# Kernel optimization log

Hardware: AMD Instinct MI355X
Metric: run time of the kernel (lower is better)

The kernel has to match this reference:

```python
import jax, jax.numpy as jnp
import numpy as np


def setup_inputs() -> dict:
    key = jax.random.key(0)
    k1, k2 = jax.random.split(key)
    B, N, P = 8, 16384, 2048
    xyz = jax.random.uniform(k1, (B, N, 3), dtype=jnp.float32)
    center_xyz = jax.random.uniform(k2, (B, P, 3), dtype=jnp.float32)
    return {
        "xyz": xyz,
        "center_xyz": center_xyz,
        "max_radius": jnp.float32(0.2),
        "sample_num": 32,
    }


def reference(xyz, center_xyz, max_radius, sample_num):
    # xyz: [B, N, 3], center_xyz: [B, P, 3] -> idx: [B, P, sample_num] int32
    B, P, _ = center_xyz.shape
    N = xyz.shape[1]
    S = int(sample_num)

    # squared distances via ||c||^2 + ||x||^2 - 2 c.x (avoids [B,P,N,3] temp)
    xn = jnp.sum(xyz * xyz, axis=-1)                      # [B, N]
    cn = jnp.sum(center_xyz * center_xyz, axis=-1)        # [B, P]
    dot = jnp.einsum("bpd,bnd->bpn", center_xyz, xyz)     # [B, P, N]
    d2 = cn[:, :, None] + xn[:, None, :] - 2.0 * dot       # [B, P, N]

    mask = d2 < (max_radius * max_radius)                  # dist < r  <=>  dist^2 < r^2
    # rank of each point among the valid ones (in index order), as in torch.where order
    rank = jnp.cumsum(mask.astype(jnp.int32), axis=-1) - 1 # [B, P, N]
    take = mask & (rank < S)
    # valid points write into slot=rank; everything else into dump slot S (discarded)
    slot = jnp.where(take, rank, S)                        # [B, P, N]

    buf = jnp.zeros((B, P, S + 1), dtype=jnp.int32)        # zeros match torch init fill
    bi = jnp.arange(B)[:, None, None]
    pi = jnp.arange(P)[None, :, None]
    src = jnp.broadcast_to(jnp.arange(N, dtype=jnp.int32), (B, P, N))
    buf = buf.at[bi, pi, slot].set(src)
    return buf[:, :, :S]
```

## Files before the change

kernel.cpp:

```cpp
#include <hip/hip_runtime.h>
#include <hip/hip_bf16.h>


__global__ __launch_bounds__(256) void ball_query_kernel(
    const float* __restrict__ xyz,
    const float* __restrict__ center,
    const float* __restrict__ p_radius,
    const int*   __restrict__ p_sample,
    int* __restrict__ out,
    int B, int N, int P)
{
    const int S = p_sample[0];
    const float r = p_radius[0];
    const float r2 = __fmul_rn(r, r);

    const int wave_id = (blockIdx.x * blockDim.x + threadIdx.x) >> 6;
    const int lane = threadIdx.x & 63;
    const int total_waves = B * P;
    if (wave_id >= total_waves) return;

    const int b = wave_id / P;
    const int p = wave_id - b * P;

    const float cx = center[(size_t)(b * P + p) * 3 + 0];
    const float cy = center[(size_t)(b * P + p) * 3 + 1];
    const float cz = center[(size_t)(b * P + p) * 3 + 2];
    const float cn = __builtin_fmaf(cz, cz,
                      __builtin_fmaf(cy, cy, __fmul_rn(cx, cx)));

    const float* xb = xyz + (size_t)b * N * 3;
    int* ob = out + (size_t)(b * P + p) * S;

    int cnt = 0;
    for (int n0 = 0; n0 < N && cnt < S; n0 += 256) {
        float px[4], py[4], pz[4];
#pragma unroll
        for (int j = 0; j < 4; ++j) {
            const int n = n0 + j * 64 + lane;
            px[j] = xb[(size_t)n * 3 + 0];
            py[j] = xb[(size_t)n * 3 + 1];
            pz[j] = xb[(size_t)n * 3 + 2];
        }
#pragma unroll
        for (int j = 0; j < 4; ++j) {
            const float x = px[j], y = py[j], z = pz[j];
            const float xn = __builtin_fmaf(z, z,
                              __builtin_fmaf(y, y, __fmul_rn(x, x)));
            const float dot = __builtin_fmaf(cz, z,
                               __builtin_fmaf(cy, y, __fmul_rn(cx, x)));
            const float d2 = __fsub_rn(__fadd_rn(cn, xn), __fmul_rn(2.0f, dot));

            const bool valid = d2 < r2;
            const unsigned long long m = __ballot(valid);
            const int rank = __builtin_amdgcn_mbcnt_hi(
                (unsigned)(m >> 32),
                __builtin_amdgcn_mbcnt_lo((unsigned)m, 0u));
            if (valid && (cnt + rank) < S) {
                ob[cnt + rank] = n0 + j * 64 + lane;
            }
            cnt += __popcll(m);
        }
    }

    if (cnt > S) cnt = S;
    for (int s = cnt + lane; s < S; s += 64) {
        ob[s] = 0;
    }
}

extern "C" void kernel_launch(void* const* d_in, const int* in_sizes, int n_in,
                              void* d_out, int out_size, void* d_ws, size_t ws_size,
                              hipStream_t stream) {
    const float* xyz      = (const float*)d_in[0];
    const float* center   = (const float*)d_in[1];
    const float* p_radius = (const float*)d_in[2];
    const int*   p_sample = (const int*)d_in[3];

    const int B = 8;
    const int N = in_sizes[0] / (B * 3);
    const int P = in_sizes[1] / (B * 3);

    int* out = (int*)d_out;

    const int total_waves = B * P;
    const int threads = 256;
    const int blocks = (total_waves * 64 + threads - 1) / threads;

    ball_query_kernel<<<blocks, threads, 0, stream>>>(
        xyz, center, p_radius, p_sample, out, B, N, P);
}
```

Measured before the change: 83.92 us.

## Double-buffer point loads with 8-chunk register prefetch in ball query

Widens each iteration from 4 to 8 point chunks per wave (512 points). It adds two register buffers so the next 512-point block is loaded while the current one is processed. The goal is to hide global-memory latency in the serial early-exit scan. In exchange it uses more registers and may load points past the early-exit point. The tail handling assumes N is a multiple of 512.

```diff
diff --git a/kernel.cpp b/kernel.cpp
--- a/kernel.cpp
+++ b/kernel.cpp
@@ -32,18 +32,25 @@
     int* ob = out + (size_t)(b * P + p) * S;
 
     int cnt = 0;
-    for (int n0 = 0; n0 < N && cnt < S; n0 += 256) {
-        float px[4], py[4], pz[4];
+
+    float Ax[8], Ay[8], Az[8];
+    float Bx[8], By[8], Bz[8];
+
+    auto load8 = [&](float (&X)[8], float (&Y)[8], float (&Z)[8], int m0) {
+        const float* q = xb + (size_t)(m0 + lane) * 3;
 #pragma unroll
-        for (int j = 0; j < 4; ++j) {
-            const int n = n0 + j * 64 + lane;
-            px[j] = xb[(size_t)n * 3 + 0];
-            py[j] = xb[(size_t)n * 3 + 1];
-            pz[j] = xb[(size_t)n * 3 + 2];
+        for (int j = 0; j < 8; ++j) {
+            X[j] = q[j * 192 + 0];
+            Y[j] = q[j * 192 + 1];
+            Z[j] = q[j * 192 + 2];
         }
+    };
+
+    auto process8 = [&](const float (&X)[8], const float (&Y)[8],
+                        const float (&Z)[8], int m0) -> bool {
 #pragma unroll
-        for (int j = 0; j < 4; ++j) {
-            const float x = px[j], y = py[j], z = pz[j];
+        for (int j = 0; j < 8; ++j) {
+            const float x = X[j], y = Y[j], z = Z[j];
             const float xn = __builtin_fmaf(z, z,
                               __builtin_fmaf(y, y, __fmul_rn(x, x)));
             const float dot = __builtin_fmaf(cz, z,
@@ -56,10 +63,24 @@
                 (unsigned)(m >> 32),
                 __builtin_amdgcn_mbcnt_lo((unsigned)m, 0u));
             if (valid && (cnt + rank) < S) {
-                ob[cnt + rank] = n0 + j * 64 + lane;
+                ob[cnt + rank] = m0 + j * 64 + lane;
             }
             cnt += __popcll(m);
         }
+        return cnt >= S;
+    };
+
+    load8(Ax, Ay, Az, 0);
+    int n0 = 0;
+    while (true) {
+        if (n0 + 1024 <= N) load8(Bx, By, Bz, n0 + 512);
+        if (process8(Ax, Ay, Az, n0)) break;
+        n0 += 512;
+        if (n0 >= N) break;
+        if (n0 + 1024 <= N) load8(Ax, Ay, Az, n0 + 512);
+        if (process8(Bx, By, Bz, n0)) break;
+        n0 += 512;
+        if (n0 >= N) break;
     }
 
     if (cnt > S) cnt = S;
```

After: 87.52 us. 1.04x slower.

## Process each center with a full block using cross-wave prefix counts

Applied to the files above, without the earlier changes.

Assigns one 256-thread block per center instead of one wave, so four waves scan 1024 points per iteration and combine their hit counts through a shared-memory prefix with a barrier. This is meant to shorten the serial scan per center before 32 neighbors are found. It adds a barrier per iteration and may scan more points than needed, since the early-exit granularity is now 1024 points.

```diff
diff --git a/kernel.cpp b/kernel.cpp
--- a/kernel.cpp
+++ b/kernel.cpp
@@ -2,7 +2,7 @@
 #include <hip/hip_bf16.h>
 
 
-__global__ __launch_bounds__(256) void ball_query_kernel(
+__global__ __launch_bounds__(256) void ball_query_block(
     const float* __restrict__ xyz,
     const float* __restrict__ center,
     const float* __restrict__ p_radius,
@@ -14,33 +14,40 @@
     const float r = p_radius[0];
     const float r2 = __fmul_rn(r, r);
 
-    const int wave_id = (blockIdx.x * blockDim.x + threadIdx.x) >> 6;
+    const int c = blockIdx.x;
     const int lane = threadIdx.x & 63;
-    const int total_waves = B * P;
-    if (wave_id >= total_waves) return;
+    const int wv = threadIdx.x >> 6;
 
-    const int b = wave_id / P;
-    const int p = wave_id - b * P;
+    const int b = c / P;
 
-    const float cx = center[(size_t)(b * P + p) * 3 + 0];
-    const float cy = center[(size_t)(b * P + p) * 3 + 1];
-    const float cz = center[(size_t)(b * P + p) * 3 + 2];
+    const float cx = center[(size_t)c * 3 + 0];
+    const float cy = center[(size_t)c * 3 + 1];
+    const float cz = center[(size_t)c * 3 + 2];
     const float cn = __builtin_fmaf(cz, cz,
                       __builtin_fmaf(cy, cy, __fmul_rn(cx, cx)));
 
     const float* xb = xyz + (size_t)b * N * 3;
-    int* ob = out + (size_t)(b * P + p) * S;
+    int* ob = out + (size_t)c * S;
+
+    __shared__ int counts[2][4];
 
     int cnt = 0;
-    for (int n0 = 0; n0 < N && cnt < S; n0 += 256) {
+    int buf = 0;
+    for (int n0 = 0; n0 < N; n0 += 1024) {
+        const int base = n0 + wv * 256 + lane;
+
         float px[4], py[4], pz[4];
 #pragma unroll
         for (int j = 0; j < 4; ++j) {
-            const int n = n0 + j * 64 + lane;
+            const int n = base + j * 64;
             px[j] = xb[(size_t)n * 3 + 0];
             py[j] = xb[(size_t)n * 3 + 1];
             pz[j] = xb[(size_t)n * 3 + 2];
         }
+
+        unsigned long long mm[4];
+        int pc[4];
+        int wtotal = 0;
 #pragma unroll
         for (int j = 0; j < 4; ++j) {
             const float x = px[j], y = py[j], z = pz[j];
@@ -49,21 +56,46 @@
             const float dot = __builtin_fmaf(cz, z,
                                __builtin_fmaf(cy, y, __fmul_rn(cx, x)));
             const float d2 = __fsub_rn(__fadd_rn(cn, xn), __fmul_rn(2.0f, dot));
+            mm[j] = __ballot(d2 < r2);
+            pc[j] = __popcll(mm[j]);
+            wtotal += pc[j];
+        }
 
-            const bool valid = d2 < r2;
-            const unsigned long long m = __ballot(valid);
+        if (lane == 0) counts[buf][wv] = wtotal;
+        __syncthreads();
+
+        const int c0 = counts[buf][0];
+        const int c1 = counts[buf][1];
+        const int c2 = counts[buf][2];
+        const int c3 = counts[buf][3];
+        int prefix = 0;
+        if (wv > 0) prefix += c0;
+        if (wv > 1) prefix += c1;
+        if (wv > 2) prefix += c2;
+        const int total = (c0 + c1) + (c2 + c3);
+
+        int off = cnt + prefix;
+#pragma unroll
+        for (int j = 0; j < 4; ++j) {
+            const unsigned long long m = mm[j];
+            const bool valid = (m >> lane) & 1ull;
             const int rank = __builtin_amdgcn_mbcnt_hi(
                 (unsigned)(m >> 32),
                 __builtin_amdgcn_mbcnt_lo((unsigned)m, 0u));
-            if (valid && (cnt + rank) < S) {
-                ob[cnt + rank] = n0 + j * 64 + lane;
+            const int slot = off + rank;
+            if (valid && slot < S) {
+                ob[slot] = base + j * 64;
             }
-            cnt += __popcll(m);
+            off += pc[j];
         }
+
+        cnt += total;
+        buf ^= 1;
+        if (cnt >= S) break;
     }
 
     if (cnt > S) cnt = S;
-    for (int s = cnt + lane; s < S; s += 64) {
+    for (int s = cnt + (int)threadIdx.x; s < S; s += 256) {
         ob[s] = 0;
     }
 }
@@ -82,10 +114,9 @@
 
     int* out = (int*)d_out;
 
-    const int total_waves = B * P;
+    const int blocks = B * P;
     const int threads = 256;
-    const int blocks = (total_waves * 64 + threads - 1) / threads;
 
-    ball_query_kernel<<<blocks, threads, 0, stream>>>(
+    ball_query_block<<<blocks, threads, 0, stream>>>(
         xyz, center, p_radius, p_sample, out, B, N, P);
 }
```

New measurement: 81.62 us. 1.03x faster.
